# Kernel tuning notes

Hardware: AMD Instinct MI355X
Metric: run time of the kernel (lower is better)

The kernel has to match this reference:

```python
import jax, jax.numpy as jnp
import numpy as np

B, NA, LAT, HID, AF, L = 512, 58, 64, 128, 10, 2
N = B * NA
E = N * 16


def silu(x):
    return x * jax.nn.sigmoid(x)


def setup_inputs() -> dict:
    key = jax.random.key(0)
    ks = list(jax.random.split(key, 32))

    def p(k, shape, fan_in):
        return jax.random.normal(k, shape, jnp.float32) / np.sqrt(fan_in)

    inp = {
        "z": jax.random.normal(ks[0], (B, LAT), jnp.float32),
        "atom_types": jax.random.uniform(ks[1], (N, AF), jnp.float32),
        "edge_index": jax.random.randint(ks[2], (2, E), 0, N, jnp.int64),
        "init_coords": jax.random.normal(ks[3], (NA, 3), jnp.float32) * 0.1,
        "latent_w": p(ks[4], (LAT, HID), LAT), "latent_b": jnp.zeros((HID,), jnp.float32),
        "atom_w": p(ks[5], (AF, HID), AF), "atom_b": jnp.zeros((HID,), jnp.float32),
        # per-layer stacked params (leading dim = num_layers)
        "edge_w1": p(ks[6], (L, 2 * HID + 1, HID), 2 * HID + 1), "edge_b1": jnp.zeros((L, HID), jnp.float32),
        "edge_w2": p(ks[7], (L, HID, HID), HID), "edge_b2": jnp.zeros((L, HID), jnp.float32),
        "node_w1": p(ks[8], (L, 2 * HID, HID), 2 * HID), "node_b1": jnp.zeros((L, HID), jnp.float32),
        "node_w2": p(ks[9], (L, HID, HID), HID), "node_b2": jnp.zeros((L, HID), jnp.float32),
        "coord_w1": p(ks[10], (L, HID, HID), HID), "coord_b1": jnp.zeros((L, HID), jnp.float32),
        "coord_w2": p(ks[11], (L, HID, 1), HID),  # no bias
        "ln_g": jnp.ones((L, HID), jnp.float32), "ln_b": jnp.zeros((L, HID), jnp.float32),
        "head_w1": p(ks[12], (HID, HID // 2), HID), "head_b1": jnp.zeros((HID // 2,), jnp.float32),
        "head_w2": p(ks[13], (HID // 2, 3), HID // 2), "head_b2": jnp.zeros((3,), jnp.float32),
    }
    return inp


def _layer(h, pos, row, col, ew1, eb1, ew2, eb2, nw1, nb1, nw2, nb2, cw1, cb1, cw2, lg, lb):
    n = h.shape[0]
    xi, xj = h[row], h[col]                      # [E,HID] gathers
    rel = pos[row] - pos[col]                    # [E,3]
    d2 = jnp.clip(jnp.sum(rel * rel, axis=-1, keepdims=True), 1e-6, 1e6)
    ef = jnp.concatenate([xi, xj, d2], axis=-1)  # [E,2H+1]
    m = silu(silu(ef @ ew1 + eb1) @ ew2 + eb2)   # edge MLP messages [E,HID]
    agg = jax.ops.segment_sum(m, row, num_segments=n)
    hn = silu(jnp.concatenate([h, agg], axis=-1) @ nw1 + nb1) @ nw2 + nb2
    mu = jnp.mean(hn, axis=-1, keepdims=True)
    var = jnp.mean((hn - mu) ** 2, axis=-1, keepdims=True)
    hn = (hn - mu) * jax.lax.rsqrt(var + 1e-5) * lg + lb
    cw = jnp.clip(silu(m @ cw1 + cb1) @ cw2, -1.0, 1.0)  # [E,1]
    upd = jax.ops.segment_sum(cw * rel, row, num_segments=n)  # [N,3]
    deg = jax.ops.segment_sum(jnp.ones((row.shape[0],), pos.dtype), row, num_segments=n)[:, None]
    pos_new = pos + upd / (deg + 1e-6)
    return hn, pos_new


def reference(z, atom_types, edge_index, init_coords, latent_w, latent_b, atom_w, atom_b,
              edge_w1, edge_b1, edge_w2, edge_b2, node_w1, node_b1, node_w2, node_b2,
              coord_w1, coord_b1, coord_w2, ln_g, ln_b, head_w1, head_b1, head_w2, head_b2):
    b = z.shape[0]
    na = init_coords.shape[0]
    n = b * na
    h = z @ latent_w + latent_b                              # [B,HID]
    h = jnp.broadcast_to(h[:, None, :], (b, na, h.shape[-1])).reshape(n, -1)
    h = h + (atom_types @ atom_w + atom_b)
    pos = jnp.broadcast_to(init_coords[None], (b, na, 3)).reshape(n, 3)
    row, col = edge_index[0], edge_index[1]
    for l in range(edge_w1.shape[0]):
        h, pos = _layer(h, pos, row, col,
                        edge_w1[l], edge_b1[l], edge_w2[l], edge_b2[l],
                        node_w1[l], node_b1[l], node_w2[l], node_b2[l],
                        coord_w1[l], coord_b1[l], coord_w2[l], ln_g[l], ln_b[l])
    delta = silu(h @ head_w1 + head_b1) @ head_w2 + head_b2
    return pos + delta
```

## Files before the change

### kernel.cpp

```cpp
#include <hip/hip_runtime.h>
#include <hip/hip_bf16.h>

#define BB 512
#define NA 58
#define LAT 64
#define HID 128
#define AF 10
#define NL 2
#define NN (BB*NA)
#define NE (NN*16)
#define ET 64
#define NTILE (NE/ET)
#define PBLK 1024

typedef __attribute__((ext_vector_type(8))) short s8;
typedef __attribute__((ext_vector_type(4))) float f4;

struct CvtDesc {
    const void* src[24];
    float*      dst[24];
    int         len[24];
};

struct PackJobs {
    const float* src[11];
    short*       dst[11];
    int          K[11];
    int          mode[11];
};

__device__ __forceinline__ float siluf(float x) {
    return x * __builtin_amdgcn_rcpf(1.0f + __expf(-x));
}

__device__ __forceinline__ short f2b(float x) {
    __hip_bfloat16 b = __float2bfloat16(x);
    return *(short*)&b;
}

__device__ __forceinline__ float b2f(short s) {
    return __uint_as_float(((unsigned int)(unsigned short)s) << 16);
}

__global__ void k_detect(const unsigned short* __restrict__ z16,
                         const unsigned int* __restrict__ e32,
                         int* __restrict__ flags) {
    __shared__ int sbf, si64;
    if (threadIdx.x == 0) { sbf = 0; si64 = 0; }
    __syncthreads();
    int c1 = 0, c2 = 0;
    for (int i = threadIdx.x; i < 1024; i += 256) {
        unsigned short v = z16[2*i];
        int e = (v >> 7) & 0xFF;
        if (e >= 100 && e <= 140) c1++;
        if (e32[2*i + 1] == 0u) c2++;
    }
    atomicAdd(&sbf, c1);
    atomicAdd(&si64, c2);
    __syncthreads();
    if (threadIdx.x == 0) {
        flags[0] = (sbf  > 600) ? 1 : 0;
        flags[1] = (si64 > 600) ? 1 : 0;
    }
}

__global__ void k_convert(CvtDesc d, const int* __restrict__ flags) {
    int a = blockIdx.y;
    int i = blockIdx.x * blockDim.x + threadIdx.x;
    int n = d.len[a];
    if (i >= n) return;
    if (flags[0]) {
        d.dst[a][i] = __bfloat162float(((const __hip_bfloat16*)d.src[a])[i]);
    } else {
        d.dst[a][i] = ((const float*)d.src[a])[i];
    }
}

__global__ void k_packall(PackJobs pj) {
    int j = blockIdx.y;
    int idx = blockIdx.x * 256 + threadIdx.x;
    const float* w = pj.src[j];
    short* o = pj.dst[j];
    int mode = pj.mode[j];
    if (mode == 0) {
        int K = pj.K[j];
        if (idx >= 128*K) return;
        int jj = idx & 7;
        int l  = (idx >> 3) & 63;
        int rest = idx >> 9;
        int KC = K >> 5;
        int kc = rest % KC;
        int nt = rest / KC;
        int n = nt*16 + (l & 15);
        int k = kc*32 + (l >> 4)*8 + jj;
        o[idx] = f2b(w[k*128 + n]);
    } else if (mode == 1) {
        if (idx >= 32768) return;
        int jj = idx & 7;
        int l  = (idx >> 3) & 63;
        int rest = idx >> 9;
        int kc = rest & 3;
        int nt = rest >> 2;
        int n = nt*16 + (l & 15);
        int k = kc*32 + (l >> 4)*8 + jj;
        float v = (n < 128) ? w[k*128 + n] : w[(128 + k)*128 + (n - 128)];
        o[idx] = f2b(v);
    } else {
        if (idx >= 8192) return;
        int jj = idx & 7;
        int l  = (idx >> 3) & 63;
        int rest = idx >> 9;
        int kc = rest & 3;
        int nt = rest >> 2;
        int n = nt*16 + (l & 15);
        int k = kc*32 + (l >> 4)*8 + jj;
        o[idx] = f2b(w[k*64 + n]);
    }
}

__global__ void k_hist(const int* __restrict__ eidx, const int* __restrict__ flags,
                       int* __restrict__ cnt) {
    int e = blockIdx.x * 256 + threadIdx.x;
    if (e >= NE) return;
    int is64 = flags[1];
    int r = eidx[is64 ? 2*(long)e : (long)e];
    atomicAdd(&cnt[r], 1);
}

__global__ __launch_bounds__(1024) void k_scan(const int* __restrict__ cnt,
                                               int* __restrict__ rowStart,
                                               int* __restrict__ cursor) {
    __shared__ int part[1024];
    int t = threadIdx.x;
    int base = t * 29;
    int loc[29];
    int s = 0;
    #pragma unroll
    for (int i = 0; i < 29; ++i) { loc[i] = s; s += cnt[base + i]; }
    part[t] = s;
    __syncthreads();
    for (int d = 1; d < 1024; d <<= 1) {
        int v = (t >= d) ? part[t - d] : 0;
        __syncthreads();
        part[t] += v;
        __syncthreads();
    }
    int pre = (t == 0) ? 0 : part[t - 1];
    #pragma unroll
    for (int i = 0; i < 29; ++i) {
        int v = pre + loc[i];
        rowStart[base + i] = v;
        cursor[base + i] = v;
    }
    if (t == 1023) rowStart[NN] = pre + s;
}

__global__ void k_scatter(const int* __restrict__ eidx, const int* __restrict__ flags,
                          int* __restrict__ cursor,
                          int* __restrict__ rS, int* __restrict__ cS) {
    int e = blockIdx.x * 256 + threadIdx.x;
    if (e >= NE) return;
    int is64 = flags[1];
    long ge = e, gc = (long)e + NE;
    int r = eidx[is64 ? 2*ge : ge];
    int c = eidx[is64 ? 2*gc : gc];
    int p = atomicAdd(&cursor[r], 1);
    rS[p] = r; cS[p] = c;
}

__global__ __launch_bounds__(256) void k_init3(
    const float* __restrict__ z, const float* __restrict__ lw,
    const float* __restrict__ lbz,
    const float* __restrict__ at,
    const float* __restrict__ aw, const float* __restrict__ ab,
    const float* __restrict__ ic,
    float* __restrict__ pos, short* __restrict__ hb,
    const short* __restrict__ wcat0, const float* __restrict__ b10,
    short* __restrict__ H1, float* __restrict__ agg, float* __restrict__ upd)
{
    __shared__ short x[64][136];
    __shared__ float awS[AF][HID];
    __shared__ float atS[64][AF+2];
    __shared__ float zbS[3][LAT];
    __shared__ float hzS[3][HID];
    const int tid = threadIdx.x;
    const int n0 = blockIdx.x * 64;
    const int b0 = n0 / NA;
    const int nb = (n0 + 63) / NA - b0 + 1;

    for (int i = tid; i < AF*HID; i += 256) awS[i/HID][i%HID] = aw[i];
    for (int i = tid; i < 64*AF; i += 256)
        atS[i/AF][i%AF] = at[(long)(n0 + i/AF)*AF + i%AF];
    for (int i = tid; i < nb*LAT; i += 256) {
        int bi = i / LAT, k = i - bi*LAT;
        int bidx = b0 + bi;
        zbS[bi][k] = (bidx < BB) ? z[bidx*LAT + k] : 0.f;
    }
    __syncthreads();

    for (int i = tid; i < nb*HID; i += 256) {
        int bi = i / HID, c = i - bi*HID;
        float acc = lbz[c];
        #pragma unroll
        for (int k = 0; k < LAT; ++k) acc += zbS[bi][k] * lw[k*HID + c];
        hzS[bi][c] = acc;
    }
    __syncthreads();

    #pragma unroll
    for (int it = 0; it < 32; ++it) {
        int idx = it*256 + tid;
        int r = idx >> 7, c = idx & 127;
        int n = n0 + r;
        float v = hzS[n/NA - b0][c] + ab[c];
        #pragma unroll
        for (int f = 0; f < AF; ++f) v += atS[r][f]*awS[f][c];
        short s = f2b(v);
        x[r][c] = s;
        hb[(long)n*HID + c] = s;
    }
    if (tid < 192) {
        int i = tid/3, d = tid - i*3;
        int n = n0 + i;
        pos[n*3 + d] = ic[(n % NA)*3 + d];
        upd[n*3 + d] = 0.f;
    }
    {
        f4* a4 = (f4*)(agg + (long)n0*HID);
        for (int j = tid; j < 64*HID/4; j += 256) a4[j] = (f4)0.f;
    }
    __syncthreads();

    const int l = tid & 63, w = tid >> 6;
    const int l16 = l & 15, quad = l >> 4;
    f4 acc[4][4];
    #pragma unroll
    for (int mt = 0; mt < 4; ++mt)
        #pragma unroll
        for (int nt4 = 0; nt4 < 4; ++nt4) acc[mt][nt4] = (f4)0.f;
    #pragma unroll
    for (int kc = 0; kc < 4; ++kc) {
        s8 a[4];
        #pragma unroll
        for (int mt = 0; mt < 4; ++mt)
            a[mt] = *(const s8*)&x[mt*16 + l16][kc*32 + quad*8];
        #pragma unroll
        for (int nt4 = 0; nt4 < 4; ++nt4) {
            int nt = w*4 + nt4;
            s8 b = *(const s8*)(wcat0 + (((size_t)nt*4 + kc)*64 + l)*8);
            #pragma unroll
            for (int mt = 0; mt < 4; ++mt)
                acc[mt][nt4] = __builtin_amdgcn_mfma_f32_16x16x32_bf16(a[mt], b, acc[mt][nt4], 0, 0, 0);
        }
    }
    #pragma unroll
    for (int nt4 = 0; nt4 < 4; ++nt4) {
        int col = (w*4 + nt4)*16 + l16;
        float bias = (col < 128) ? b10[col] : 0.f;
        #pragma unroll
        for (int mt = 0; mt < 4; ++mt)
            #pragma unroll
            for (int i = 0; i < 4; ++i) {
                int row = mt*16 + quad*4 + i;
                H1[(long)(n0 + row)*256 + col] = f2b(acc[mt][nt4][i] + bias);
            }
    }
}

__global__ __launch_bounds__(256, 3) void k_edge8(
    const short* __restrict__ H1,
    const int* __restrict__ rS, const int* __restrict__ cS,
    const float* __restrict__ pos,
    const float* __restrict__ w1c,
    const short* __restrict__ w2p, const float* __restrict__ b2,
    const short* __restrict__ c1p, const float* __restrict__ cb1,
    const float* __restrict__ cw2,
    float* __restrict__ agg, float* __restrict__ upd)
{
    __shared__ short t1[2][ET][136];
    __shared__ int   rIs[2][ET], cIs[2][ET];
    __shared__ float sred[ET];

    const int tid = threadIdx.x;
    const int l = tid & 63, w = tid >> 6;
    const int l16 = l & 15, quad = l >> 4;
    const int c0 = (2*w)*16 + l16, c1c = (2*w+1)*16 + l16;
    const int half = tid >> 7, ch = tid & 127;
    const int q = tid & 15;
    const int esub = tid >> 4;

    float wv[8];
    #pragma unroll
    for (int j = 0; j < 8; ++j) wv[j] = w1c[q*8 + j];

    s8 w2f[8], c1f[8];
    #pragma unroll
    for (int kc = 0; kc < 4; ++kc) {
        w2f[kc]     = *(const s8*)(w2p + (((size_t)(2*w)*4 + kc)*64 + l)*8);
        w2f[4 + kc] = *(const s8*)(w2p + (((size_t)(2*w+1)*4 + kc)*64 + l)*8);
        c1f[kc]     = *(const s8*)(c1p + (((size_t)(2*w)*4 + kc)*64 + l)*8);
        c1f[4 + kc] = *(const s8*)(c1p + (((size_t)(2*w+1)*4 + kc)*64 + l)*8);
    }
    const float bia2_0 = b2[c0],  bia2_1 = b2[c1c];
    const float biac_0 = cb1[c0], biac_1 = cb1[c1c];
    const float cw0    = cw2[c0], cw1v   = cw2[c1c];

    int   pri[4], pci[4];
    float pd2[4];
    auto PREIDX = [&](int T) {
        long eb = (long)T * ET;
        #pragma unroll
        for (int it = 0; it < 4; ++it) {
            int e = esub + 16*it;
            int r = rS[eb + e], c = cS[eb + e];
            pri[it] = r; pci[it] = c;
            float rx = pos[r*3+0] - pos[c*3+0];
            float ry = pos[r*3+1] - pos[c*3+1];
            float rz = pos[r*3+2] - pos[c*3+2];
            pd2[it] = fminf(fmaxf(rx*rx + ry*ry + rz*rz, 1e-6f), 1e6f);
        }
    };

    int T = blockIdx.x;
    PREIDX(T);
    #pragma unroll
    for (int it = 0; it < 4; ++it) {
        s8 va = *(const s8*)(H1 + (long)pri[it]*256 + q*8);
        s8 vb = *(const s8*)(H1 + (long)pci[it]*256 + 128 + q*8);
        float d2 = pd2[it];
        s8 o;
        #pragma unroll
        for (int j = 0; j < 8; ++j)
            o[j] = f2b(siluf(b2f(va[j]) + b2f(vb[j]) + d2*wv[j]));
        *(s8*)&t1[0][esub + 16*it][q*8] = o;
    }
    if (q == 0) {
        #pragma unroll
        for (int it = 0; it < 4; ++it) {
            rIs[0][esub + 16*it] = pri[it];
            cIs[0][esub + 16*it] = pci[it];
        }
    }
    if (tid < ET) sred[tid] = 0.f;
    int Tn = T + PBLK;
    if (Tn < NTILE) PREIDX(Tn);
    __syncthreads();

    int b = 0;
    while (true) {
        const bool hasNext = (Tn < NTILE);

        f4 acc[4][2];
        {
            #pragma unroll
            for (int mt = 0; mt < 4; ++mt) { acc[mt][0] = (f4)0.f; acc[mt][1] = (f4)0.f; }
            #pragma unroll
            for (int it = 0; it < 4; ++it) {
                s8 va, vb;
                if (hasNext) {
                    va = *(const s8*)(H1 + (long)pri[it]*256 + q*8);
                    vb = *(const s8*)(H1 + (long)pci[it]*256 + 128 + q*8);
                }
                #pragma unroll
                for (int mt = 0; mt < 4; ++mt) {
                    s8 a = *(const s8*)&t1[b][mt*16 + l16][it*32 + quad*8];
                    acc[mt][0] = __builtin_amdgcn_mfma_f32_16x16x32_bf16(a, w2f[it],     acc[mt][0], 0, 0, 0);
                    acc[mt][1] = __builtin_amdgcn_mfma_f32_16x16x32_bf16(a, w2f[4 + it], acc[mt][1], 0, 0, 0);
                }
                if (hasNext) {
                    float d2 = pd2[it];
                    s8 o;
                    #pragma unroll
                    for (int j = 0; j < 8; ++j)
                        o[j] = f2b(siluf(b2f(va[j]) + b2f(vb[j]) + d2*wv[j]));
                    *(s8*)&t1[b^1][esub + 16*it][q*8] = o;
                }
            }
            if (hasNext && q == 0) {
                #pragma unroll
                for (int it = 0; it < 4; ++it) {
                    rIs[b^1][esub + 16*it] = pri[it];
                    cIs[b^1][esub + 16*it] = pci[it];
                }
            }
        }
        __syncthreads();

        short (*mm)[136] = t1[b];
        #pragma unroll
        for (int mt = 0; mt < 4; ++mt) {
            #pragma unroll
            for (int i = 0; i < 4; ++i) {
                int row = mt*16 + quad*4 + i;
                mm[row][c0]  = f2b(siluf(acc[mt][0][i] + bia2_0));
                mm[row][c1c] = f2b(siluf(acc[mt][1][i] + bia2_1));
            }
        }
        __syncthreads();

        {
            int e0 = half * 32;
            int cur = rIs[b][e0];
            float a = 0.f;
            #pragma unroll
            for (int e = e0; e < e0 + 32; ++e) {
                int r = rIs[b][e];
                if (r != cur) {
                    atomicAdd(&agg[(long)cur*HID + ch], a);
                    a = 0.f; cur = r;
                }
                a += b2f(mm[e][ch]);
            }
            atomicAdd(&agg[(long)cur*HID + ch], a);
        }
        {
            f4 acc3[4][2];
            #pragma unroll
            for (int mt = 0; mt < 4; ++mt) { acc3[mt][0] = (f4)0.f; acc3[mt][1] = (f4)0.f; }
            #pragma unroll
            for (int kc = 0; kc < 4; ++kc) {
                #pragma unroll
                for (int mt = 0; mt < 4; ++mt) {
                    s8 a = *(const s8*)&mm[mt*16 + l16][kc*32 + quad*8];
                    acc3[mt][0] = __builtin_amdgcn_mfma_f32_16x16x32_bf16(a, c1f[kc],     acc3[mt][0], 0, 0, 0);
                    acc3[mt][1] = __builtin_amdgcn_mfma_f32_16x16x32_bf16(a, c1f[4 + kc], acc3[mt][1], 0, 0, 0);
                }
            }
            #pragma unroll
            for (int mt = 0; mt < 4; ++mt) {
                #pragma unroll
                for (int i = 0; i < 4; ++i) {
                    float p = siluf(acc3[mt][0][i] + biac_0) * cw0
                            + siluf(acc3[mt][1][i] + biac_1) * cw1v;
                    p += __shfl_xor(p, 1);
                    p += __shfl_xor(p, 2);
                    p += __shfl_xor(p, 4);
                    p += __shfl_xor(p, 8);
                    if (l16 == 0) {
                        int row = mt*16 + quad*4 + i;
                        atomicAdd(&sred[row], p);
                    }
                }
            }
        }
        int   ur = 0;
        float urx = 0.f, ury = 0.f, urz = 0.f;
        if (tid < ET) {
            ur = rIs[b][tid];
            int uc = cIs[b][tid];
            urx = pos[ur*3+0] - pos[uc*3+0];
            ury = pos[ur*3+1] - pos[uc*3+1];
            urz = pos[ur*3+2] - pos[uc*3+2];
        }
        int Tnn = Tn + PBLK;
        if (hasNext && Tnn < NTILE) PREIDX(Tnn);
        __syncthreads();

        if (tid < ET) {
            float cwv = fminf(fmaxf(sred[tid], -1.f), 1.f);
            sred[tid] = 0.f;
            atomicAdd(&upd[ur*3+0], cwv*urx);
            atomicAdd(&upd[ur*3+1], cwv*ury);
            atomicAdd(&upd[ur*3+2], cwv*urz);
        }
        if (!hasNext) break;
        T = Tn; Tn = Tnn; b ^= 1;
    }
}

__global__ __launch_bounds__(256) void k_node_mfma(
    short* __restrict__ hb, float* __restrict__ agg,
    const short* __restrict__ w1p, const float* __restrict__ b1n,
    const short* __restrict__ w2p, const float* __restrict__ b2n,
    const float* __restrict__ lg, const float* __restrict__ lb,
    float* __restrict__ pos, float* __restrict__ upd,
    const int* __restrict__ rowStart,
    const short* __restrict__ wcatn, const float* __restrict__ b1next,
    short* __restrict__ H1,
    const short* __restrict__ hw1p, const float* __restrict__ hb1,
    const float* __restrict__ hw2, const float* __restrict__ hb2,
    void* __restrict__ out, const int* __restrict__ flags)
{
    __shared__ short x[64][264];
    __shared__ short t1[64][144];
    __shared__ float mus[64], rstds[64];
    __shared__ float posS[64][3];
    float (*hn)[132] = (float (*)[132])&x[0][0];
    float (*hid)[68] = (float (*)[68])&x[0][0];

    const int tid = threadIdx.x;
    const int n0 = blockIdx.x * 64;

    #pragma unroll
    for (int it = 0; it < 4; ++it) {
        int idx = it*256 + tid;
        int e = idx >> 4, qq = idx & 15;
        *(int4*)&x[e][qq*8] = *(const int4*)(hb + (long)(n0+e)*HID + qq*8);
    }
    #pragma unroll
    for (int it = 0; it < 8; ++it) {
        int idx = it*256 + tid;
        int e = idx >> 5, qq = idx & 31;
        float4 v = *(const float4*)(agg + (long)(n0+e)*HID + qq*4);
        short4 sv;
        sv.x = f2b(v.x); sv.y = f2b(v.y); sv.z = f2b(v.z); sv.w = f2b(v.w);
        *(short4*)&x[e][128 + qq*4] = sv;
    }
    __syncthreads();

    {
        f4* a4 = (f4*)(agg + (long)n0*HID);
        for (int j = tid; j < 64*HID/4; j += 256) a4[j] = (f4)0.f;
    }

    const int l = tid & 63, w = tid >> 6;
    const int l16 = l & 15, quad = l >> 4;
    const int nt0 = 2*w, nt1 = 2*w + 1;
    const int c0 = nt0*16 + l16, c1c = nt1*16 + l16;

    {
        f4 acc[4][2];
        #pragma unroll
        for (int mt = 0; mt < 4; ++mt) { acc[mt][0] = (f4)0.f; acc[mt][1] = (f4)0.f; }
        #pragma unroll
        for (int kc = 0; kc < 8; ++kc) {
            s8 b0  = *(const s8*)(w1p + (((size_t)nt0*8 + kc)*64 + l)*8);
            s8 b1f = *(const s8*)(w1p + (((size_t)nt1*8 + kc)*64 + l)*8);
            #pragma unroll
            for (int mt = 0; mt < 4; ++mt) {
                s8 a = *(const s8*)&x[mt*16 + l16][kc*32 + quad*8];
                acc[mt][0] = __builtin_amdgcn_mfma_f32_16x16x32_bf16(a, b0,  acc[mt][0], 0, 0, 0);
                acc[mt][1] = __builtin_amdgcn_mfma_f32_16x16x32_bf16(a, b1f, acc[mt][1], 0, 0, 0);
            }
        }
        float bia0 = b1n[c0], bia1 = b1n[c1c];
        #pragma unroll
        for (int mt = 0; mt < 4; ++mt) {
            #pragma unroll
            for (int i = 0; i < 4; ++i) {
                int row = mt*16 + quad*4 + i;
                t1[row][c0]  = f2b(siluf(acc[mt][0][i] + bia0));
                t1[row][c1c] = f2b(siluf(acc[mt][1][i] + bia1));
            }
        }
    }
    __syncthreads();

    {
        f4 acc[4][2];
        #pragma unroll
        for (int mt = 0; mt < 4; ++mt) { acc[mt][0] = (f4)0.f; acc[mt][1] = (f4)0.f; }
        #pragma unroll
        for (int kc = 0; kc < 4; ++kc) {
            s8 b0  = *(const s8*)(w2p + (((size_t)nt0*4 + kc)*64 + l)*8);
            s8 b1f = *(const s8*)(w2p + (((size_t)nt1*4 + kc)*64 + l)*8);
            #pragma unroll
            for (int mt = 0; mt < 4; ++mt) {
                s8 a = *(const s8*)&t1[mt*16 + l16][kc*32 + quad*8];
                acc[mt][0] = __builtin_amdgcn_mfma_f32_16x16x32_bf16(a, b0,  acc[mt][0], 0, 0, 0);
                acc[mt][1] = __builtin_amdgcn_mfma_f32_16x16x32_bf16(a, b1f, acc[mt][1], 0, 0, 0);
            }
        }
        float bia0 = b2n[c0], bia1 = b2n[c1c];
        __syncthreads();
        #pragma unroll
        for (int mt = 0; mt < 4; ++mt) {
            #pragma unroll
            for (int i = 0; i < 4; ++i) {
                int row = mt*16 + quad*4 + i;
                hn[row][c0]  = acc[mt][0][i] + bia0;
                hn[row][c1c] = acc[mt][1][i] + bia1;
            }
        }
    }
    __syncthreads();

    {
        int r = tid >> 2, part = tid & 3;
        float s = 0.f, qv = 0.f;
        #pragma unroll
        for (int j = 0; j < 32; ++j) {
            float v = hn[r][part + 4*j];
            s += v; qv += v*v;
        }
        s += __shfl_xor(s, 1); qv += __shfl_xor(qv, 1);
        s += __shfl_xor(s, 2); qv += __shfl_xor(qv, 2);
        if (part == 0) {
            float mu = s * (1.0f/HID);
            float var = qv * (1.0f/HID) - mu*mu;
            mus[r] = mu;
            rstds[r] = rsqrtf(var + 1e-5f);
        }
    }
    __syncthreads();

    #pragma unroll
    for (int it = 0; it < 32; ++it) {
        int idx = it*256 + tid;
        int r = idx >> 7, c = idx & 127;
        float v = (hn[r][c] - mus[r]) * rstds[r] * lg[c] + lb[c];
        short s = f2b(v);
        hb[(long)(n0 + r)*HID + c] = s;
        t1[r][c] = s;
    }
    if (tid < 192) {
        int i = tid / 3, d = tid - i*3;
        int n = n0 + i;
        float dg = (float)(rowStart[n+1] - rowStart[n]);
        float np = pos[n*3+d] + upd[n*3+d] / (dg + 1e-6f);
        pos[n*3+d] = np;
        posS[i][d] = np;
        upd[n*3+d] = 0.f;
    }
    __syncthreads();

    if (wcatn) {
        f4 acc[4][4];
        #pragma unroll
        for (int mt = 0; mt < 4; ++mt)
            #pragma unroll
            for (int nt4 = 0; nt4 < 4; ++nt4) acc[mt][nt4] = (f4)0.f;
        #pragma unroll
        for (int kc = 0; kc < 4; ++kc) {
            s8 a[4];
            #pragma unroll
            for (int mt = 0; mt < 4; ++mt)
                a[mt] = *(const s8*)&t1[mt*16 + l16][kc*32 + quad*8];
            #pragma unroll
            for (int nt4 = 0; nt4 < 4; ++nt4) {
                int nt = w*4 + nt4;
                s8 b = *(const s8*)(wcatn + (((size_t)nt*4 + kc)*64 + l)*8);
                #pragma unroll
                for (int mt = 0; mt < 4; ++mt)
                    acc[mt][nt4] = __builtin_amdgcn_mfma_f32_16x16x32_bf16(a[mt], b, acc[mt][nt4], 0, 0, 0);
            }
        }
        #pragma unroll
        for (int nt4 = 0; nt4 < 4; ++nt4) {
            int col = (w*4 + nt4)*16 + l16;
            float bias = (col < 128) ? b1next[col] : 0.f;
            #pragma unroll
            for (int mt = 0; mt < 4; ++mt)
                #pragma unroll
                for (int i = 0; i < 4; ++i) {
                    int row = mt*16 + quad*4 + i;
                    H1[(long)(n0 + row)*256 + col] = f2b(acc[mt][nt4][i] + bias);
                }
        }
    } else {
        f4 acc[4];
        #pragma unroll
        for (int mt = 0; mt < 4; ++mt) acc[mt] = (f4)0.f;
        #pragma unroll
        for (int kc = 0; kc < 4; ++kc) {
            s8 b = *(const s8*)(hw1p + (((size_t)w*4 + kc)*64 + l)*8);
            #pragma unroll
            for (int mt = 0; mt < 4; ++mt) {
                s8 a = *(const s8*)&t1[mt*16 + l16][kc*32 + quad*8];
                acc[mt] = __builtin_amdgcn_mfma_f32_16x16x32_bf16(a, b, acc[mt], 0, 0, 0);
            }
        }
        int col = w*16 + l16;
        float bias = hb1[col];
        #pragma unroll
        for (int mt = 0; mt < 4; ++mt)
            #pragma unroll
            for (int i = 0; i < 4; ++i) {
                int row = mt*16 + quad*4 + i;
                hid[row][col] = siluf(acc[mt][i] + bias);
            }
        __syncthreads();
        if (tid < 192) {
            int r = tid / 3, cc = tid - r*3;
            float a2 = hb2[cc];
            #pragma unroll
            for (int k = 0; k < 64; ++k) a2 += hid[r][k] * hw2[k*3 + cc];
            int n = n0 + r;
            float v = posS[r][cc] + a2;
            if (flags[0]) ((__hip_bfloat16*)out)[n*3+cc] = __float2bfloat16(v);
            else          ((float*)out)[n*3+cc] = v;
        }
    }
}

extern "C" void kernel_launch(void* const* d_in, const int* in_sizes, int n_in,
                              void* d_out, int out_size, void* d_ws, size_t ws_size,
                              hipStream_t stream)
{
    (void)in_sizes; (void)n_in; (void)out_size; (void)ws_size;

    int* flags = (int*)d_ws;
    float* base = (float*)d_ws;
    size_t off = 64;
    auto alloc = [&](size_t n) { float* p = base + off; off += (n + 63) & ~63ull; return p; };

    static const int aidx[24] = {0,1,3,4,5,6,7,8,9,10,11,12,13,14,15,16,17,18,19,20,21,22,23,24};
    static const int alen[24] = {
        BB*LAT, NN*AF, NA*3, LAT*HID, HID, AF*HID, HID,
        NL*257*HID, NL*HID, NL*HID*HID, NL*HID,
        NL*256*HID, NL*HID, NL*HID*HID, NL*HID,
        NL*HID*HID, NL*HID, NL*HID, NL*HID, NL*HID,
        HID*64, 64, 64*3, 3
    };
    CvtDesc cd;
    float* fp[24];
    for (int a = 0; a < 24; ++a) {
        fp[a] = alloc((size_t)alen[a]);
        cd.src[a] = d_in[aidx[a]];
        cd.dst[a] = fp[a];
        cd.len[a] = alen[a];
    }
    float* agg = alloc((size_t)NN*HID);
    float* pos = alloc((size_t)NN*3);
    float* upd = alloc((size_t)NN*3);
    short* hb  = (short*)alloc((size_t)NN*HID/2);
    short* H1  = (short*)alloc((size_t)NN*256/2);
    short* wcatp = (short*)alloc((size_t)NL*32768/2);
    short* w2p = (short*)alloc((size_t)NL*16384/2);
    short* c1p = (short*)alloc((size_t)NL*16384/2);
    short* nw1p = (short*)alloc((size_t)NL*32768/2);
    short* nw2p = (short*)alloc((size_t)NL*16384/2);
    short* hw1p = (short*)alloc((size_t)8192/2);
    int* cnt      = (int*)alloc((size_t)NN);
    int* rowStart = (int*)alloc((size_t)NN + 1);
    int* cursor   = (int*)alloc((size_t)NN);
    int* rS       = (int*)alloc((size_t)NE);
    int* cS       = (int*)alloc((size_t)NE);
    const int* eidx = (const int*)d_in[2];

    k_detect<<<1, 256, 0, stream>>>((const unsigned short*)d_in[0],
                                    (const unsigned int*)d_in[2], flags);
    k_convert<<<dim3((NN*AF + 255)/256, 24), 256, 0, stream>>>(cd, flags);

    PackJobs pj;
    for (int l = 0; l < NL; ++l) {
        int b5 = l*5;
        pj.src[b5+0] = fp[7]  + (size_t)l*257*HID; pj.dst[b5+0] = wcatp + (size_t)l*32768; pj.K[b5+0] = 256; pj.mode[b5+0] = 1;
        pj.src[b5+1] = fp[9]  + (size_t)l*HID*HID; pj.dst[b5+1] = w2p   + (size_t)l*16384; pj.K[b5+1] = 128; pj.mode[b5+1] = 0;
        pj.src[b5+2] = fp[15] + (size_t)l*HID*HID; pj.dst[b5+2] = c1p   + (size_t)l*16384; pj.K[b5+2] = 128; pj.mode[b5+2] = 0;
        pj.src[b5+3] = fp[11] + (size_t)l*256*HID; pj.dst[b5+3] = nw1p  + (size_t)l*32768; pj.K[b5+3] = 256; pj.mode[b5+3] = 0;
        pj.src[b5+4] = fp[13] + (size_t)l*HID*HID; pj.dst[b5+4] = nw2p  + (size_t)l*16384; pj.K[b5+4] = 128; pj.mode[b5+4] = 0;
    }
    pj.src[10] = fp[20]; pj.dst[10] = hw1p; pj.K[10] = 128; pj.mode[10] = 2;
    k_packall<<<dim3(128, 11), 256, 0, stream>>>(pj);

    hipMemsetAsync(cnt, 0, (size_t)NN*sizeof(int), stream);
    k_hist<<<(NE + 255)/256, 256, 0, stream>>>(eidx, flags, cnt);
    k_scan<<<1, 1024, 0, stream>>>(cnt, rowStart, cursor);
    k_scatter<<<(NE + 255)/256, 256, 0, stream>>>(eidx, flags, cursor, rS, cS);

    k_init3<<<NN/64, 256, 0, stream>>>(fp[0], fp[3], fp[4],
                                       fp[1], fp[5], fp[6], fp[2], pos, hb,
                                       wcatp, fp[8], H1, agg, upd);

    for (int l = 0; l < NL; ++l) {
        k_edge8<<<PBLK, 256, 0, stream>>>(H1, rS, cS, pos,
            fp[7] + (size_t)l*257*HID + 256*HID,
            w2p + (size_t)l*16384, fp[10] + (size_t)l*HID,
            c1p + (size_t)l*16384, fp[16] + (size_t)l*HID,
            fp[17] + (size_t)l*HID,
            agg, upd);
        const short* wcatn = (l+1 < NL) ? (wcatp + (size_t)(l+1)*32768) : nullptr;
        const float* b1nx  = (l+1 < NL) ? (fp[8] + (size_t)(l+1)*HID) : fp[8];
        k_node_mfma<<<NN/64, 256, 0, stream>>>(hb, agg,
            nw1p + (size_t)l*32768, fp[12] + (size_t)l*HID,
            nw2p + (size_t)l*16384, fp[14] + (size_t)l*HID,
            fp[18] + (size_t)l*HID, fp[19] + (size_t)l*HID,
            pos, upd, rowStart, wcatn, b1nx, H1,
            hw1p, fp[21], fp[22], fp[23], d_out, flags);
    }
}
```

Baseline: 689.7 us.

## Replace persistent double-buffered edge kernel with one-tile-per-block launch

The edge kernel no longer runs as a persistent grid of 1024 blocks looping over tiles with a double-buffered gather/compute pipeline. It now launches one block per 64-edge tile (NTILE blocks), each gathering, running both MFMA stages, and scattering once. This drops the software prefetch and loop overhead and leaves latency hiding to hardware occupancy across many blocks. The cost is reloading the per-block weight fragments in every block and losing explicit overlap of gathers with MFMA work.

Result: faster. 599.3 us (-13.1%).

```diff
diff --git a/kernel.cpp b/kernel.cpp
--- a/kernel.cpp
+++ b/kernel.cpp
@@ -11,7 +11,6 @@
 #define NE (NN*16)
 #define ET 64
 #define NTILE (NE/ET)
-#define PBLK 1024
 
 typedef __attribute__((ext_vector_type(8))) short s8;
 typedef __attribute__((ext_vector_type(4))) float f4;
@@ -267,7 +266,7 @@
     }
 }
 
-__global__ __launch_bounds__(256, 3) void k_edge8(
+__global__ __launch_bounds__(256, 3) void k_edge_os(
     const short* __restrict__ H1,
     const int* __restrict__ rS, const int* __restrict__ cS,
     const float* __restrict__ pos,
@@ -277,8 +276,9 @@
     const float* __restrict__ cw2,
     float* __restrict__ agg, float* __restrict__ upd)
 {
-    __shared__ short t1[2][ET][136];
-    __shared__ int   rIs[2][ET], cIs[2][ET];
+    __shared__ short t1[ET][136];
+    __shared__ short mm[ET][136];
+    __shared__ int   rIs[ET], cIs[ET];
     __shared__ float sred[ET];
 
     const int tid = threadIdx.x;
@@ -288,6 +288,7 @@
     const int half = tid >> 7, ch = tid & 127;
     const int q = tid & 15;
     const int esub = tid >> 4;
+    const int T = blockIdx.x;
 
     float wv[8];
     #pragma unroll
@@ -305,88 +306,40 @@
     const float biac_0 = cb1[c0], biac_1 = cb1[c1c];
     const float cw0    = cw2[c0], cw1v   = cw2[c1c];
 
-    int   pri[4], pci[4];
-    float pd2[4];
-    auto PREIDX = [&](int T) {
-        long eb = (long)T * ET;
-        #pragma unroll
-        for (int it = 0; it < 4; ++it) {
-            int e = esub + 16*it;
-            int r = rS[eb + e], c = cS[eb + e];
-            pri[it] = r; pci[it] = c;
-            float rx = pos[r*3+0] - pos[c*3+0];
-            float ry = pos[r*3+1] - pos[c*3+1];
-            float rz = pos[r*3+2] - pos[c*3+2];
-            pd2[it] = fminf(fmaxf(rx*rx + ry*ry + rz*rz, 1e-6f), 1e6f);
-        }
-    };
-
-    int T = blockIdx.x;
-    PREIDX(T);
+    const long eb = (long)T * ET;
+    if (tid < ET) sred[tid] = 0.f;
     #pragma unroll
     for (int it = 0; it < 4; ++it) {
-        s8 va = *(const s8*)(H1 + (long)pri[it]*256 + q*8);
-        s8 vb = *(const s8*)(H1 + (long)pci[it]*256 + 128 + q*8);
-        float d2 = pd2[it];
+        int e = esub + 16*it;
+        int r = rS[eb + e], c = cS[eb + e];
+        float rx = pos[r*3+0] - pos[c*3+0];
+        float ry = pos[r*3+1] - pos[c*3+1];
+        float rz = pos[r*3+2] - pos[c*3+2];
+        float d2 = fminf(fmaxf(rx*rx + ry*ry + rz*rz, 1e-6f), 1e6f);
+        s8 va = *(const s8*)(H1 + (long)r*256 + q*8);
+        s8 vb = *(const s8*)(H1 + (long)c*256 + 128 + q*8);
         s8 o;
         #pragma unroll
         for (int j = 0; j < 8; ++j)
             o[j] = f2b(siluf(b2f(va[j]) + b2f(vb[j]) + d2*wv[j]));
-        *(s8*)&t1[0][esub + 16*it][q*8] = o;
-    }
-    if (q == 0) {
+        *(s8*)&t1[e][q*8] = o;
+        if (q == 0) { rIs[e] = r; cIs[e] = c; }
+    }
+    __syncthreads();
+
+    {
+        f4 acc[4][2];
+        #pragma unroll
+        for (int mt = 0; mt < 4; ++mt) { acc[mt][0] = (f4)0.f; acc[mt][1] = (f4)0.f; }
         #pragma unroll
         for (int it = 0; it < 4; ++it) {
-            rIs[0][esub + 16*it] = pri[it];
-            cIs[0][esub + 16*it] = pci[it];
-        }
-    }
-    if (tid < ET) sred[tid] = 0.f;
-    int Tn = T + PBLK;
-    if (Tn < NTILE) PREIDX(Tn);
-    __syncthreads();
-
-    int b = 0;
-    while (true) {
-        const bool hasNext = (Tn < NTILE);
-
-        f4 acc[4][2];
-        {
-            #pragma unroll
-            for (int mt = 0; mt < 4; ++mt) { acc[mt][0] = (f4)0.f; acc[mt][1] = (f4)0.f; }
-            #pragma unroll
-            for (int it = 0; it < 4; ++it) {
-                s8 va, vb;
-                if (hasNext) {
-                    va = *(const s8*)(H1 + (long)pri[it]*256 + q*8);
-                    vb = *(const s8*)(H1 + (long)pci[it]*256 + 128 + q*8);
-                }
-                #pragma unroll
-                for (int mt = 0; mt < 4; ++mt) {
-                    s8 a = *(const s8*)&t1[b][mt*16 + l16][it*32 + quad*8];
-                    acc[mt][0] = __builtin_amdgcn_mfma_f32_16x16x32_bf16(a, w2f[it],     acc[mt][0], 0, 0, 0);
-                    acc[mt][1] = __builtin_amdgcn_mfma_f32_16x16x32_bf16(a, w2f[4 + it], acc[mt][1], 0, 0, 0);
-                }
-                if (hasNext) {
-                    float d2 = pd2[it];
-                    s8 o;
-                    #pragma unroll
-                    for (int j = 0; j < 8; ++j)
-                        o[j] = f2b(siluf(b2f(va[j]) + b2f(vb[j]) + d2*wv[j]));
-                    *(s8*)&t1[b^1][esub + 16*it][q*8] = o;
-                }
-            }
-            if (hasNext && q == 0) {
-                #pragma unroll
-                for (int it = 0; it < 4; ++it) {
-                    rIs[b^1][esub + 16*it] = pri[it];
-                    cIs[b^1][esub + 16*it] = pci[it];
-                }
-            }
-        }
-        __syncthreads();
-
-        short (*mm)[136] = t1[b];
+            #pragma unroll
+            for (int mt = 0; mt < 4; ++mt) {
+                s8 a = *(const s8*)&t1[mt*16 + l16][it*32 + quad*8];
+                acc[mt][0] = __builtin_amdgcn_mfma_f32_16x16x32_bf16(a, w2f[it],     acc[mt][0], 0, 0, 0);
+                acc[mt][1] = __builtin_amdgcn_mfma_f32_16x16x32_bf16(a, w2f[4 + it], acc[mt][1], 0, 0, 0);
+            }
+        }
         #pragma unroll
         for (int mt = 0; mt < 4; ++mt) {
             #pragma unroll
@@ -396,75 +349,70 @@
                 mm[row][c1c] = f2b(siluf(acc[mt][1][i] + bia2_1));
             }
         }
-        __syncthreads();
-
-        {
-            int e0 = half * 32;
-            int cur = rIs[b][e0];
-            float a = 0.f;
-            #pragma unroll
-            for (int e = e0; e < e0 + 32; ++e) {
-                int r = rIs[b][e];
-                if (r != cur) {
-                    atomicAdd(&agg[(long)cur*HID + ch], a);
-                    a = 0.f; cur = r;
+    }
+    __syncthreads();
+
+    {
+        int e0 = half * 32;
+        int cur = rIs[e0];
+        float a = 0.f;
+        #pragma unroll
+        for (int e = e0; e < e0 + 32; ++e) {
+            int r = rIs[e];
+            if (r != cur) {
+                atomicAdd(&agg[(long)cur*HID + ch], a);
+                a = 0.f; cur = r;
+            }
+            a += b2f(mm[e][ch]);
+        }
+        atomicAdd(&agg[(long)cur*HID + ch], a);
+    }
+    {
+        f4 acc3[4][2];
+        #pragma unroll
+        for (int mt = 0; mt < 4; ++mt) { acc3[mt][0] = (f4)0.f; acc3[mt][1] = (f4)0.f; }
+        #pragma unroll
+        for (int kc = 0; kc < 4; ++kc) {
+            #pragma unroll
+            for (int mt = 0; mt < 4; ++mt) {
+                s8 a = *(const s8*)&mm[mt*16 + l16][kc*32 + quad*8];
+                acc3[mt][0] = __builtin_amdgcn_mfma_f32_16x16x32_bf16(a, c1f[kc],     acc3[mt][0], 0, 0, 0);
+                acc3[mt][1] = __builtin_amdgcn_mfma_f32_16x16x32_bf16(a, c1f[4 + kc], acc3[mt][1], 0, 0, 0);
+            }
+        }
+        #pragma unroll
+        for (int mt = 0; mt < 4; ++mt) {
+            #pragma unroll
+            for (int i = 0; i < 4; ++i) {
+                float p = siluf(acc3[mt][0][i] + biac_0) * cw0
+                        + siluf(acc3[mt][1][i] + biac_1) * cw1v;
+                p += __shfl_xor(p, 1);
+                p += __shfl_xor(p, 2);
+                p += __shfl_xor(p, 4);
+                p += __shfl_xor(p, 8);
+                if (l16 == 0) {
+                    int row = mt*16 + quad*4 + i;
+                    atomicAdd(&sred[row], p);
                 }
-                a += b2f(mm[e][ch]);
-            }
-            atomicAdd(&agg[(long)cur*HID + ch], a);
-        }
-        {
-            f4 acc3[4][2];
-            #pragma unroll
-            for (int mt = 0; mt < 4; ++mt) { acc3[mt][0] = (f4)0.f; acc3[mt][1] = (f4)0.f; }
-            #pragma unroll
-            for (int kc = 0; kc < 4; ++kc) {
-                #pragma unroll
-                for (int mt = 0; mt < 4; ++mt) {
-                    s8 a = *(const s8*)&mm[mt*16 + l16][kc*32 + quad*8];
-                    acc3[mt][0] = __builtin_amdgcn_mfma_f32_16x16x32_bf16(a, c1f[kc],     acc3[mt][0], 0, 0, 0);
-                    acc3[mt][1] = __builtin_amdgcn_mfma_f32_16x16x32_bf16(a, c1f[4 + kc], acc3[mt][1], 0, 0, 0);
-                }
-            }
-            #pragma unroll
-            for (int mt = 0; mt < 4; ++mt) {
-                #pragma unroll
-                for (int i = 0; i < 4; ++i) {
-                    float p = siluf(acc3[mt][0][i] + biac_0) * cw0
-                            + siluf(acc3[mt][1][i] + biac_1) * cw1v;
-                    p += __shfl_xor(p, 1);
-                    p += __shfl_xor(p, 2);
-                    p += __shfl_xor(p, 4);
-                    p += __shfl_xor(p, 8);
-                    if (l16 == 0) {
-                        int row = mt*16 + quad*4 + i;
-                        atomicAdd(&sred[row], p);
-                    }
-                }
-            }
-        }
-        int   ur = 0;
-        float urx = 0.f, ury = 0.f, urz = 0.f;
-        if (tid < ET) {
-            ur = rIs[b][tid];
-            int uc = cIs[b][tid];
-            urx = pos[ur*3+0] - pos[uc*3+0];
-            ury = pos[ur*3+1] - pos[uc*3+1];
-            urz = pos[ur*3+2] - pos[uc*3+2];
-        }
-        int Tnn = Tn + PBLK;
-        if (hasNext && Tnn < NTILE) PREIDX(Tnn);
-        __syncthreads();
-
-        if (tid < ET) {
-            float cwv = fminf(fmaxf(sred[tid], -1.f), 1.f);
-            sred[tid] = 0.f;
-            atomicAdd(&upd[ur*3+0], cwv*urx);
-            atomicAdd(&upd[ur*3+1], cwv*ury);
-            atomicAdd(&upd[ur*3+2], cwv*urz);
-        }
-        if (!hasNext) break;
-        T = Tn; Tn = Tnn; b ^= 1;
+            }
+        }
+    }
+    int   ur = 0;
+    float urx = 0.f, ury = 0.f, urz = 0.f;
+    if (tid < ET) {
+        ur = rIs[tid];
+        int uc = cIs[tid];
+        urx = pos[ur*3+0] - pos[uc*3+0];
+        ury = pos[ur*3+1] - pos[uc*3+1];
+        urz = pos[ur*3+2] - pos[uc*3+2];
+    }
+    __syncthreads();
+
+    if (tid < ET) {
+        float cwv = fminf(fmaxf(sred[tid], -1.f), 1.f);
+        atomicAdd(&upd[ur*3+0], cwv*urx);
+        atomicAdd(&upd[ur*3+1], cwv*ury);
+        atomicAdd(&upd[ur*3+2], cwv*urz);
     }
 }
 
@@ -754,7 +702,7 @@
                                        wcatp, fp[8], H1, agg, upd);
 
     for (int l = 0; l < NL; ++l) {
-        k_edge8<<<PBLK, 256, 0, stream>>>(H1, rS, cS, pos,
+        k_edge_os<<<NTILE, 256, 0, stream>>>(H1, rS, cS, pos,
             fp[7] + (size_t)l*257*HID + 256*HID,
             w2p + (size_t)l*16384, fp[10] + (size_t)l*HID,
             c1p + (size_t)l*16384, fp[16] + (size_t)l*HID,
```
